# Kernel tuning notes

Measured on AMD Instinct MI355X. Metric: run time of the kernel, lower is better.

The kernel has to match this reference:

```python
import jax, jax.numpy as jnp
import numpy as np

H = 8  # number of heads


def setup_inputs() -> dict:
    key0 = jax.random.key(0)
    ks = jax.random.split(key0, 10)
    B, Lq, Lk = 2, 256, 512
    q_model = k_model = v_model = d_model = 512
    d_k = d_model // H
    s = 0.02
    return {
        "query": jax.random.normal(ks[0], (B, Lq, q_model), jnp.float32),
        "key": jax.random.normal(ks[1], (B, Lk, k_model), jnp.float32),
        "value": jax.random.normal(ks[2], (B, Lk, v_model), jnp.float32),
        "mask": jax.random.randint(ks[3], (B, Lk), 0, 2, jnp.int32),
        # weights stored as (in, out) so projection is x @ W
        "Wq": jax.random.normal(ks[4], (q_model, d_model), jnp.float32) * s,
        "Wk": jax.random.normal(ks[5], (k_model, d_model), jnp.float32) * s,
        "Wv": jax.random.normal(ks[6], (v_model, d_model), jnp.float32) * s,
        "Wo": jax.random.normal(ks[7], (d_model, d_model), jnp.float32) * s,
        "wa": jax.random.normal(ks[8], (d_k,), jnp.float32) * s,
    }


def reference(query, key, value, mask, Wq, Wk, Wv, Wo, wa):
    B, Lq, _ = query.shape
    Lk = key.shape[1]
    d_model = Wq.shape[1]
    d_k = d_model // H

    def split_heads(x, W, L):
        return (x @ W).reshape(B, L, H, d_k).transpose(0, 2, 1, 3)  # (B,H,L,dk)

    q = split_heads(query, Wq, Lq)
    k = split_heads(key, Wk, Lk)
    v = split_heads(value, Wv, Lk)

    # additive (Bahdanau) scores: tanh(q_i + k_j) . wa  -> (B,H,Lq,Lk)
    feats = jnp.tanh(q[:, :, :, None, :] + k[:, :, None, :, :])
    scores = jnp.einsum("bhqkd,d->bhqk", feats, wa)

    scores = jnp.where(mask[:, None, None, :] == 0, jnp.float32(-1e9), scores)
    weights = jax.nn.softmax(scores, axis=-1)

    x = jnp.einsum("bhqk,bhkd->bhqd", weights, v)
    x = x.transpose(0, 2, 1, 3).reshape(B, Lq, H * d_k)
    return x @ Wo
```

## Files before the change

kernel.cpp:

```cpp
#include <hip/hip_runtime.h>

#define NB 2
#define LQ 256
#define LK 512
#define DM 512
#define NH 8
#define C2F 2.885390081777927f
#define L2E 1.4426950408889634f

typedef __attribute__((ext_vector_type(8))) short short8;
typedef __attribute__((ext_vector_type(4))) float f32x4;

__device__ __forceinline__ ushort f2bf(float x) {
    unsigned int u = __float_as_uint(x);
    unsigned int r = (u + 0x7fffu + ((u >> 16) & 1u)) >> 16;
    return (ushort)r;
}
__device__ __forceinline__ float bf2f(ushort u) {
    return __uint_as_float(((unsigned int)u) << 16);
}

__global__ __launch_bounds__(256) void prep_kernel(
    const float* __restrict__ query, const float* __restrict__ key,
    const float* __restrict__ value, const int* __restrict__ mask,
    const float* __restrict__ Wq, const float* __restrict__ Wk,
    const float* __restrict__ Wv, const float* __restrict__ Wo,
    ushort* __restrict__ Ah, ushort* __restrict__ Al,
    ushort* __restrict__ Wth, ushort* __restrict__ Wtl,
    int* __restrict__ vidx, int* __restrict__ nvarr)
{
    __shared__ float T[32][33];
    const int blk = blockIdx.x;
    const int tid = threadIdx.x;

    if (blk < 1280) {
        int i = (blk * 256 + tid) * 4;
        const float* src;
        if (i < 262144)       src = query + i;
        else if (i < 786432)  src = key + (i - 262144);
        else                  src = value + (i - 786432);
        float4 x = *reinterpret_cast<const float4*>(src);
        ushort h0 = f2bf(x.x), h1 = f2bf(x.y), h2 = f2bf(x.z), h3 = f2bf(x.w);
        *reinterpret_cast<ushort4*>(&Ah[i]) = make_ushort4(h0, h1, h2, h3);
        *reinterpret_cast<ushort4*>(&Al[i]) = make_ushort4(
            f2bf(x.x - bf2f(h0)), f2bf(x.y - bf2f(h1)),
            f2bf(x.z - bf2f(h2)), f2bf(x.w - bf2f(h3)));
    } else if (blk < 2304) {
        const int bid2 = blk - 1280;
        const int widx = bid2 >> 8;
        const int kt = (bid2 >> 4) & 15, nt = bid2 & 15;
        const float* W = (widx == 0) ? Wq : (widx == 1) ? Wk : (widx == 2) ? Wv : Wo;
        const int rr = tid >> 3, c4 = tid & 7;
        float4 v = *reinterpret_cast<const float4*>(&W[(size_t)(kt * 32 + rr) * 512 + nt * 32 + c4 * 4]);
        T[c4 * 4 + 0][rr] = v.x;
        T[c4 * 4 + 1][rr] = v.y;
        T[c4 * 4 + 2][rr] = v.z;
        T[c4 * 4 + 3][rr] = v.w;
        __syncthreads();
        const int nr = tid >> 3, k4 = tid & 7;
        float x0 = T[nr][k4 * 4 + 0], x1 = T[nr][k4 * 4 + 1];
        float x2 = T[nr][k4 * 4 + 2], x3 = T[nr][k4 * 4 + 3];
        ushort h0 = f2bf(x0), h1 = f2bf(x1), h2 = f2bf(x2), h3 = f2bf(x3);
        size_t o = (size_t)widx * 262144 + (size_t)(nt * 32 + nr) * 512 + kt * 32 + k4 * 4;
        *reinterpret_cast<ushort4*>(&Wth[o]) = make_ushort4(h0, h1, h2, h3);
        *reinterpret_cast<ushort4*>(&Wtl[o]) = make_ushort4(
            f2bf(x0 - bf2f(h0)), f2bf(x1 - bf2f(h1)), f2bf(x2 - bf2f(h2)), f2bf(x3 - bf2f(h3)));
    } else {
        const int b = blk - 2304;
        if (tid < 64) {
            const int lane = tid;
            const int* mb = mask + b * LK;
            int base = 0;
            #pragma unroll
            for (int it = 0; it < 8; ++it) {
                int j = it * 64 + lane;
                bool m = mb[j] != 0;
                unsigned long long bal = __ballot(m);
                int pos = base + (int)__popcll(bal & ((1ull << lane) - 1ull));
                if (m) vidx[b * 512 + pos] = j;
                base += (int)__popcll(bal);
            }
            for (int j = base + lane; j < 512; j += 64) vidx[b * 512 + j] = 0;
            if (lane == 0) nvarr[b] = base;
        }
    }
}

__device__ __forceinline__ void wave_gemm16(
    const ushort* __restrict__ Ah, const ushort* __restrict__ Al, int arow0,
    const ushort* __restrict__ Bth, const ushort* __restrict__ Btl, int ncol0,
    float* __restrict__ C, int crow0, float scale, int lane)
{
    const int fr = lane & 15, k8 = (lane >> 4) * 8;
    const ushort* aph = Ah + (size_t)(arow0 + fr) * 512 + k8;
    const ushort* apl = Al + (size_t)(arow0 + fr) * 512 + k8;
    const ushort* bph = Bth + (size_t)(ncol0 + fr) * 512 + k8;
    const ushort* bpl = Btl + (size_t)(ncol0 + fr) * 512 + k8;
    f32x4 acc = (f32x4)0.0f;
    #pragma unroll 4
    for (int k0 = 0; k0 < 512; k0 += 32) {
        short8 a_h = *reinterpret_cast<const short8*>(aph + k0);
        short8 a_l = *reinterpret_cast<const short8*>(apl + k0);
        short8 b_h = *reinterpret_cast<const short8*>(bph + k0);
        short8 b_l = *reinterpret_cast<const short8*>(bpl + k0);
        acc = __builtin_amdgcn_mfma_f32_16x16x32_bf16(a_h, b_h, acc, 0, 0, 0);
        acc = __builtin_amdgcn_mfma_f32_16x16x32_bf16(a_h, b_l, acc, 0, 0, 0);
        acc = __builtin_amdgcn_mfma_f32_16x16x32_bf16(a_l, b_h, acc, 0, 0, 0);
    }
    #pragma unroll
    for (int i = 0; i < 4; ++i)
        C[(size_t)(crow0 + (lane >> 4) * 4 + i) * 512 + ncol0 + fr] = acc[i] * scale;
}

__global__ __launch_bounds__(256) void qkv_gemm_kernel(
    const ushort* __restrict__ Ah, const ushort* __restrict__ Al,
    const ushort* __restrict__ Wth, const ushort* __restrict__ Wtl,
    float* __restrict__ Qb, float* __restrict__ Kb, float* __restrict__ Vb)
{
    const int gw = (blockIdx.x * 256 + threadIdx.x) >> 6;
    const int lane = threadIdx.x & 63;
    const int mt = gw >> 5, nt = gw & 31;
    const ushort* bth; const ushort* btl; float* C; int crow0; float scale;
    if (mt < 32)      { bth = Wth;          btl = Wtl;          C = Qb; crow0 = mt * 16;        scale = C2F; }
    else if (mt < 96) { bth = Wth + 262144; btl = Wtl + 262144; C = Kb; crow0 = (mt - 32) * 16; scale = C2F; }
    else              { bth = Wth + 524288; btl = Wtl + 524288; C = Vb; crow0 = (mt - 96) * 16; scale = 1.0f; }
    wave_gemm16(Ah, Al, mt * 16, bth, btl, nt * 16, C, crow0, scale, lane);
}

__global__ __launch_bounds__(256) void out_gemm_kernel(
    const ushort* __restrict__ xh, const ushort* __restrict__ xl,
    const ushort* __restrict__ Woh, const ushort* __restrict__ Wol,
    float* __restrict__ out)
{
    const int gw = (blockIdx.x * 256 + threadIdx.x) >> 6;
    const int lane = threadIdx.x & 63;
    const int mt = gw >> 5, nt = gw & 31;
    wave_gemm16(xh, xl, mt * 16, Woh, Wol, nt * 16, out, mt * 16, 1.0f, lane);
}

#define SCOP(QV, KV, WV, U) { \
    float e_ = __builtin_amdgcn_exp2f((QV) + (KV)); \
    float r_ = __builtin_amdgcn_rcpf(1.0f + e_); \
    (U) = fmaf((WV), r_, (U)); }

__global__ __launch_bounds__(256) void attn_kernel(
    const float* __restrict__ Qb, const float* __restrict__ Kb,
    const float* __restrict__ Vb, const float* __restrict__ wa,
    const int* __restrict__ vidx, const int* __restrict__ nvarr,
    ushort* __restrict__ xh, ushort* __restrict__ xl)
{
    __shared__ float qs[2][64];
    __shared__ float was[64];
    __shared__ float wsm[2][512];
    __shared__ float red[2][8];
    __shared__ float xp[4][2][64];
    __shared__ int vlds[512];
    __shared__ int nv_s;

    const int tid = threadIdx.x;
    const int lane = tid & 63;
    const int w = tid >> 6;
    const int bid = blockIdx.x;
    const int qt = bid & 127;
    const int h = (bid >> 7) & 7;
    const int b = bid >> 10;
    const int q0 = qt * 2;

    if (tid < 128) {
        int r = tid >> 6, d = tid & 63;
        qs[r][d] = Qb[(size_t)(b * LQ + q0 + r) * DM + h * 64 + d];
    }
    if (tid < 64) was[tid] = wa[tid];
    vlds[tid] = vidx[b * 512 + tid];
    vlds[tid + 256] = vidx[b * 512 + tid + 256];
    if (tid == 0) nv_s = nvarr[b];
    __syncthreads();
    const int nv = nv_s;

    float swa = was[lane];
    #pragma unroll
    for (int off = 32; off > 0; off >>= 1) swa += __shfl_xor(swa, off);

    const float* Kh = Kb + ((size_t)b * LK) * DM + h * 64;
    float s[2][2];

    #pragma unroll
    for (int c = 0; c < 2; ++c) {
        const int sbase = c * 256 + w * 64;
        if (sbase >= nv) { s[0][c] = -1e9f; s[1][c] = -1e9f; continue; }
        const int slot = sbase + lane;
        const bool act = slot < nv;
        const int row = vlds[slot];
        const float* Kp = Kh + (size_t)row * DM;
        float u0 = 0.0f, u1 = 0.0f;
        #pragma unroll
        for (int db = 0; db < 8; ++db) {
            const int d0 = db * 8;
            float4 kA = *reinterpret_cast<const float4*>(&Kp[d0]);
            float4 kB = *reinterpret_cast<const float4*>(&Kp[d0 + 4]);
            float4 qA0 = *reinterpret_cast<const float4*>(&qs[0][d0]);
            float4 qB0 = *reinterpret_cast<const float4*>(&qs[0][d0 + 4]);
            float4 qA1 = *reinterpret_cast<const float4*>(&qs[1][d0]);
            float4 qB1 = *reinterpret_cast<const float4*>(&qs[1][d0 + 4]);
            float4 wA = *reinterpret_cast<const float4*>(&was[d0]);
            float4 wB = *reinterpret_cast<const float4*>(&was[d0 + 4]);
            SCOP(qA0.x, kA.x, wA.x, u0)  SCOP(qA1.x, kA.x, wA.x, u1)
            SCOP(qA0.y, kA.y, wA.y, u0)  SCOP(qA1.y, kA.y, wA.y, u1)
            SCOP(qA0.z, kA.z, wA.z, u0)  SCOP(qA1.z, kA.z, wA.z, u1)
            SCOP(qA0.w, kA.w, wA.w, u0)  SCOP(qA1.w, kA.w, wA.w, u1)
            SCOP(qB0.x, kB.x, wB.x, u0)  SCOP(qB1.x, kB.x, wB.x, u1)
            SCOP(qB0.y, kB.y, wB.y, u0)  SCOP(qB1.y, kB.y, wB.y, u1)
            SCOP(qB0.z, kB.z, wB.z, u0)  SCOP(qB1.z, kB.z, wB.z, u1)
            SCOP(qB0.w, kB.w, wB.w, u0)  SCOP(qB1.w, kB.w, wB.w, u1)
        }
        s[0][c] = act ? fmaf(-2.0f, u0, swa) : -1e9f;
        s[1][c] = act ? fmaf(-2.0f, u1, swa) : -1e9f;
    }

    #pragma unroll
    for (int r = 0; r < 2; ++r) {
        float mx = fmaxf(s[r][0], s[r][1]);
        #pragma unroll
        for (int off = 32; off > 0; off >>= 1) mx = fmaxf(mx, __shfl_xor(mx, off));
        if (lane == 0) red[r][w] = mx;
    }
    __syncthreads();
    float p[2][2];
    #pragma unroll
    for (int r = 0; r < 2; ++r) {
        float gmx = fmaxf(fmaxf(red[r][0], red[r][1]), fmaxf(red[r][2], red[r][3]));
        p[r][0] = __builtin_amdgcn_exp2f((s[r][0] - gmx) * L2E);
        p[r][1] = __builtin_amdgcn_exp2f((s[r][1] - gmx) * L2E);
        float sm = p[r][0] + p[r][1];
        #pragma unroll
        for (int off = 32; off > 0; off >>= 1) sm += __shfl_xor(sm, off);
        if (lane == 0) red[r][4 + w] = sm;
    }
    __syncthreads();
    #pragma unroll
    for (int r = 0; r < 2; ++r) {
        float tot = (red[r][4] + red[r][5]) + (red[r][6] + red[r][7]);
        float inv = __builtin_amdgcn_rcpf(tot);
        wsm[r][w * 64 + lane] = p[r][0] * inv;
        wsm[r][256 + w * 64 + lane] = p[r][1] * inv;
    }
    __syncthreads();

    const float* Vh = Vb + ((size_t)b * LK) * DM + h * 64;
    float o0 = 0.0f, o1 = 0.0f;
    const int ngr = (nv + 3) >> 2;
    for (int gi = w; gi < ngr; gi += 4) {
        const int sb = gi * 4;
        float4 w0 = *reinterpret_cast<const float4*>(&wsm[0][sb]);
        float4 w1 = *reinterpret_cast<const float4*>(&wsm[1][sb]);
        int j0 = vlds[sb + 0], j1 = vlds[sb + 1], j2 = vlds[sb + 2], j3 = vlds[sb + 3];
        float v0 = Vh[(size_t)j0 * DM + lane];
        float v1 = Vh[(size_t)j1 * DM + lane];
        float v2 = Vh[(size_t)j2 * DM + lane];
        float v3 = Vh[(size_t)j3 * DM + lane];
        o0 = fmaf(w0.x, v0, o0); o0 = fmaf(w0.y, v1, o0);
        o0 = fmaf(w0.z, v2, o0); o0 = fmaf(w0.w, v3, o0);
        o1 = fmaf(w1.x, v0, o1); o1 = fmaf(w1.y, v1, o1);
        o1 = fmaf(w1.z, v2, o1); o1 = fmaf(w1.w, v3, o1);
    }
    xp[w][0][lane] = o0;
    xp[w][1][lane] = o1;
    __syncthreads();
    if (w < 2) {
        const int r = w;
        float acc = (xp[0][r][lane] + xp[1][r][lane]) + (xp[2][r][lane] + xp[3][r][lane]);
        size_t oidx = (size_t)(b * LQ + q0 + r) * DM + h * 64 + lane;
        ushort hb = f2bf(acc);
        xh[oidx] = hb;
        xl[oidx] = f2bf(acc - bf2f(hb));
    }
}

extern "C" void kernel_launch(void* const* d_in, const int* in_sizes, int n_in,
                              void* d_out, int out_size, void* d_ws, size_t ws_size,
                              hipStream_t stream)
{
    const float* query = (const float*)d_in[0];
    const float* key   = (const float*)d_in[1];
    const float* value = (const float*)d_in[2];
    const int*   mask  = (const int*)d_in[3];
    const float* Wq    = (const float*)d_in[4];
    const float* Wk    = (const float*)d_in[5];
    const float* Wv    = (const float*)d_in[6];
    const float* Wo    = (const float*)d_in[7];
    const float* wa    = (const float*)d_in[8];
    float* out = (float*)d_out;

    char* W = (char*)d_ws;
    float*  Qb    = (float*)(W);
    float*  Kb    = (float*)(W + 1048576);
    float*  Vb    = (float*)(W + 3145728);
    ushort* Ah    = (ushort*)(W + 5242880);
    ushort* Al    = (ushort*)(W + 7864320);
    ushort* Wth   = (ushort*)(W + 10485760);
    ushort* Wtl   = (ushort*)(W + 12582912);
    ushort* xh    = (ushort*)(W + 14680064);
    ushort* xl    = (ushort*)(W + 15204352);
    int*    vidx  = (int*)(W + 15728640);
    int*    nvarr = (int*)(W + 15732736);

    prep_kernel<<<dim3(2306), 256, 0, stream>>>(query, key, value, mask,
                                                Wq, Wk, Wv, Wo, Ah, Al, Wth, Wtl, vidx, nvarr);
    qkv_gemm_kernel<<<dim3(1280), 256, 0, stream>>>(Ah, Al, Wth, Wtl, Qb, Kb, Vb);
    attn_kernel<<<dim3(2048), 256, 0, stream>>>(Qb, Kb, Vb, wa, vidx, nvarr, xh, xl);
    out_gemm_kernel<<<dim3(256), 256, 0, stream>>>(xh, xl, Wth + 786432, Wtl + 786432, out);
}
```

Before: 161.8 us.

## Tile GEMMs through LDS, compact K/V in epilogue, process four query rows per block

The projection and output GEMMs now compute 64x64 tiles per block, staging bf16 hi/lo operands in shared memory, where before each wave computed an independent 16x16 tile straight from global memory. The QKV GEMM epilogue scatters K and V rows directly into a compacted layout that holds only unmasked keys, using an inverse position map built in prep, so attention reads K and V contiguously with no index indirection. The attention kernel handles four query rows per block instead of two, reusing each loaded K/V row across more queries and halving the block count. The trade-offs are a much smaller GEMM grid (64 blocks for the output projection) and added synchronisation in the K loop.

```diff
diff --git a/kernel.cpp b/kernel.cpp
--- a/kernel.cpp
+++ b/kernel.cpp
@@ -5,6 +5,7 @@
 #define LK 512
 #define DM 512
 #define NH 8
+#define ROWS 4
 #define C2F 2.885390081777927f
 #define L2E 1.4426950408889634f
 
@@ -27,7 +28,7 @@
     const float* __restrict__ Wv, const float* __restrict__ Wo,
     ushort* __restrict__ Ah, ushort* __restrict__ Al,
     ushort* __restrict__ Wth, ushort* __restrict__ Wtl,
-    int* __restrict__ vidx, int* __restrict__ nvarr)
+    int* __restrict__ pinv, int* __restrict__ nvarr)
 {
     __shared__ float T[32][33];
     const int blk = blockIdx.x;
@@ -77,54 +78,109 @@
                 bool m = mb[j] != 0;
                 unsigned long long bal = __ballot(m);
                 int pos = base + (int)__popcll(bal & ((1ull << lane) - 1ull));
-                if (m) vidx[b * 512 + pos] = j;
+                pinv[b * 512 + j] = m ? pos : -1;
                 base += (int)__popcll(bal);
             }
-            for (int j = base + lane; j < 512; j += 64) vidx[b * 512 + j] = 0;
             if (lane == 0) nvarr[b] = base;
         }
     }
 }
 
-__device__ __forceinline__ void wave_gemm16(
+__device__ __forceinline__ void gemm64_acc(
     const ushort* __restrict__ Ah, const ushort* __restrict__ Al, int arow0,
-    const ushort* __restrict__ Bth, const ushort* __restrict__ Btl, int ncol0,
-    float* __restrict__ C, int crow0, float scale, int lane)
-{
-    const int fr = lane & 15, k8 = (lane >> 4) * 8;
-    const ushort* aph = Ah + (size_t)(arow0 + fr) * 512 + k8;
-    const ushort* apl = Al + (size_t)(arow0 + fr) * 512 + k8;
-    const ushort* bph = Bth + (size_t)(ncol0 + fr) * 512 + k8;
-    const ushort* bpl = Btl + (size_t)(ncol0 + fr) * 512 + k8;
-    f32x4 acc = (f32x4)0.0f;
-    #pragma unroll 4
+    const ushort* __restrict__ Bth, const ushort* __restrict__ Btl, int col0,
+    f32x4 (&acc)[2][2])
+{
+    __shared__ __align__(16) ushort AsH[64 * 40];
+    __shared__ __align__(16) ushort AsL[64 * 40];
+    __shared__ __align__(16) ushort BsH[64 * 40];
+    __shared__ __align__(16) ushort BsL[64 * 40];
+    const int tid = threadIdx.x;
+    const int lane = tid & 63;
+    const int w = tid >> 6, wr = w >> 1, wc = w & 1;
+    const int srow = tid >> 2, sk8 = (tid & 3) * 8;
+
+    #pragma unroll
+    for (int i = 0; i < 2; ++i)
+        #pragma unroll
+        for (int j = 0; j < 2; ++j) acc[i][j] = (f32x4)0.0f;
+
+    const int fr_row = (lane & 15), fk8 = (lane >> 4) * 8;
+
     for (int k0 = 0; k0 < 512; k0 += 32) {
-        short8 a_h = *reinterpret_cast<const short8*>(aph + k0);
-        short8 a_l = *reinterpret_cast<const short8*>(apl + k0);
-        short8 b_h = *reinterpret_cast<const short8*>(bph + k0);
-        short8 b_l = *reinterpret_cast<const short8*>(bpl + k0);
-        acc = __builtin_amdgcn_mfma_f32_16x16x32_bf16(a_h, b_h, acc, 0, 0, 0);
-        acc = __builtin_amdgcn_mfma_f32_16x16x32_bf16(a_h, b_l, acc, 0, 0, 0);
-        acc = __builtin_amdgcn_mfma_f32_16x16x32_bf16(a_l, b_h, acc, 0, 0, 0);
-    }
-    #pragma unroll
-    for (int i = 0; i < 4; ++i)
-        C[(size_t)(crow0 + (lane >> 4) * 4 + i) * 512 + ncol0 + fr] = acc[i] * scale;
+        short8 gah = *reinterpret_cast<const short8*>(&Ah[(size_t)(arow0 + srow) * 512 + k0 + sk8]);
+        short8 gal = *reinterpret_cast<const short8*>(&Al[(size_t)(arow0 + srow) * 512 + k0 + sk8]);
+        short8 gbh = *reinterpret_cast<const short8*>(&Bth[(size_t)(col0 + srow) * 512 + k0 + sk8]);
+        short8 gbl = *reinterpret_cast<const short8*>(&Btl[(size_t)(col0 + srow) * 512 + k0 + sk8]);
+        __syncthreads();
+        *reinterpret_cast<short8*>(&AsH[srow * 40 + sk8]) = gah;
+        *reinterpret_cast<short8*>(&AsL[srow * 40 + sk8]) = gal;
+        *reinterpret_cast<short8*>(&BsH[srow * 40 + sk8]) = gbh;
+        *reinterpret_cast<short8*>(&BsL[srow * 40 + sk8]) = gbl;
+        __syncthreads();
+        short8 ah[2], al[2], bh[2], bl[2];
+        #pragma unroll
+        for (int fr = 0; fr < 2; ++fr) {
+            int r = wr * 32 + fr * 16 + fr_row;
+            ah[fr] = *reinterpret_cast<const short8*>(&AsH[r * 40 + fk8]);
+            al[fr] = *reinterpret_cast<const short8*>(&AsL[r * 40 + fk8]);
+        }
+        #pragma unroll
+        for (int fc = 0; fc < 2; ++fc) {
+            int n = wc * 32 + fc * 16 + fr_row;
+            bh[fc] = *reinterpret_cast<const short8*>(&BsH[n * 40 + fk8]);
+            bl[fc] = *reinterpret_cast<const short8*>(&BsL[n * 40 + fk8]);
+        }
+        #pragma unroll
+        for (int fr = 0; fr < 2; ++fr)
+            #pragma unroll
+            for (int fc = 0; fc < 2; ++fc) {
+                acc[fr][fc] = __builtin_amdgcn_mfma_f32_16x16x32_bf16(ah[fr], bh[fc], acc[fr][fc], 0, 0, 0);
+                acc[fr][fc] = __builtin_amdgcn_mfma_f32_16x16x32_bf16(ah[fr], bl[fc], acc[fr][fc], 0, 0, 0);
+                acc[fr][fc] = __builtin_amdgcn_mfma_f32_16x16x32_bf16(al[fr], bh[fc], acc[fr][fc], 0, 0, 0);
+            }
+    }
 }
 
 __global__ __launch_bounds__(256) void qkv_gemm_kernel(
     const ushort* __restrict__ Ah, const ushort* __restrict__ Al,
     const ushort* __restrict__ Wth, const ushort* __restrict__ Wtl,
-    float* __restrict__ Qb, float* __restrict__ Kb, float* __restrict__ Vb)
-{
-    const int gw = (blockIdx.x * 256 + threadIdx.x) >> 6;
+    const int* __restrict__ pinv,
+    float* __restrict__ Qb, float* __restrict__ Kc, float* __restrict__ Vc)
+{
+    const int rb = blockIdx.y, cb = blockIdx.x;
+    const int row0 = rb * 64, col0 = cb * 64;
+    const ushort* bth; const ushort* btl;
+    if (rb < 8)       { bth = Wth;          btl = Wtl; }
+    else if (rb < 24) { bth = Wth + 262144; btl = Wtl + 262144; }
+    else              { bth = Wth + 524288; btl = Wtl + 524288; }
+    f32x4 acc[2][2];
+    gemm64_acc(Ah, Al, row0, bth, btl, col0, acc);
     const int lane = threadIdx.x & 63;
-    const int mt = gw >> 5, nt = gw & 31;
-    const ushort* bth; const ushort* btl; float* C; int crow0; float scale;
-    if (mt < 32)      { bth = Wth;          btl = Wtl;          C = Qb; crow0 = mt * 16;        scale = C2F; }
-    else if (mt < 96) { bth = Wth + 262144; btl = Wtl + 262144; C = Kb; crow0 = (mt - 32) * 16; scale = C2F; }
-    else              { bth = Wth + 524288; btl = Wtl + 524288; C = Vb; crow0 = (mt - 96) * 16; scale = 1.0f; }
-    wave_gemm16(Ah, Al, mt * 16, bth, btl, nt * 16, C, crow0, scale, lane);
+    const int w = threadIdx.x >> 6, wr = w >> 1, wc = w & 1;
+    #pragma unroll
+    for (int fr = 0; fr < 2; ++fr)
+        #pragma unroll
+        for (int fc = 0; fc < 2; ++fc)
+            #pragma unroll
+            for (int i = 0; i < 4; ++i) {
+                int r = row0 + wr * 32 + fr * 16 + (lane >> 4) * 4 + i;
+                int c = col0 + wc * 32 + fc * 16 + (lane & 15);
+                float v = acc[fr][fc][i];
+                if (r < 512) {
+                    Qb[(size_t)r * 512 + c] = v * C2F;
+                } else if (r < 1536) {
+                    int rk = r - 512;
+                    int pos = pinv[rk];
+                    if (pos >= 0)
+                        Kc[(size_t)((rk >> 9) * 512 + pos) * 512 + c] = v * C2F;
+                } else {
+                    int rv = r - 1536;
+                    int pos = pinv[rv];
+                    if (pos >= 0)
+                        Vc[(size_t)((rv >> 9) * 512 + pos) * 512 + c] = v;
+                }
+            }
 }
 
 __global__ __launch_bounds__(256) void out_gemm_kernel(
@@ -132,10 +188,21 @@
     const ushort* __restrict__ Woh, const ushort* __restrict__ Wol,
     float* __restrict__ out)
 {
-    const int gw = (blockIdx.x * 256 + threadIdx.x) >> 6;
+    const int row0 = blockIdx.y * 64, col0 = blockIdx.x * 64;
+    f32x4 acc[2][2];
+    gemm64_acc(xh, xl, row0, Woh, Wol, col0, acc);
     const int lane = threadIdx.x & 63;
-    const int mt = gw >> 5, nt = gw & 31;
-    wave_gemm16(xh, xl, mt * 16, Woh, Wol, nt * 16, out, mt * 16, 1.0f, lane);
+    const int w = threadIdx.x >> 6, wr = w >> 1, wc = w & 1;
+    #pragma unroll
+    for (int fr = 0; fr < 2; ++fr)
+        #pragma unroll
+        for (int fc = 0; fc < 2; ++fc)
+            #pragma unroll
+            for (int i = 0; i < 4; ++i) {
+                int r = row0 + wr * 32 + fr * 16 + (lane >> 4) * 4 + i;
+                int c = col0 + wc * 32 + fc * 16 + (lane & 15);
+                out[(size_t)r * 512 + c] = acc[fr][fc][i];
+            }
 }
 
 #define SCOP(QV, KV, WV, U) { \
@@ -144,35 +211,32 @@
     (U) = fmaf((WV), r_, (U)); }
 
 __global__ __launch_bounds__(256) void attn_kernel(
-    const float* __restrict__ Qb, const float* __restrict__ Kb,
-    const float* __restrict__ Vb, const float* __restrict__ wa,
-    const int* __restrict__ vidx, const int* __restrict__ nvarr,
+    const float* __restrict__ Qb, const float* __restrict__ Kc,
+    const float* __restrict__ Vc, const float* __restrict__ wa,
+    const int* __restrict__ nvarr,
     ushort* __restrict__ xh, ushort* __restrict__ xl)
 {
-    __shared__ float qs[2][64];
+    __shared__ float qs[ROWS][64];
     __shared__ float was[64];
-    __shared__ float wsm[2][512];
-    __shared__ float red[2][8];
-    __shared__ float xp[4][2][64];
-    __shared__ int vlds[512];
+    __shared__ float wsm[ROWS][512];
+    __shared__ float red[ROWS][8];
+    __shared__ float xp[4][ROWS][64];
     __shared__ int nv_s;
 
     const int tid = threadIdx.x;
     const int lane = tid & 63;
     const int w = tid >> 6;
     const int bid = blockIdx.x;
-    const int qt = bid & 127;
-    const int h = (bid >> 7) & 7;
-    const int b = bid >> 10;
-    const int q0 = qt * 2;
-
-    if (tid < 128) {
+    const int qt = bid & 63;
+    const int h = (bid >> 6) & 7;
+    const int b = bid >> 9;
+    const int q0 = qt * ROWS;
+
+    {
         int r = tid >> 6, d = tid & 63;
         qs[r][d] = Qb[(size_t)(b * LQ + q0 + r) * DM + h * 64 + d];
     }
     if (tid < 64) was[tid] = wa[tid];
-    vlds[tid] = vidx[b * 512 + tid];
-    vlds[tid + 256] = vidx[b * 512 + tid + 256];
     if (tid == 0) nv_s = nvarr[b];
     __syncthreads();
     const int nv = nv_s;
@@ -181,53 +245,58 @@
     #pragma unroll
     for (int off = 32; off > 0; off >>= 1) swa += __shfl_xor(swa, off);
 
-    const float* Kh = Kb + ((size_t)b * LK) * DM + h * 64;
-    float s[2][2];
+    const float* Kh = Kc + ((size_t)b * LK) * DM + h * 64;
+    float s[ROWS][2];
 
     #pragma unroll
     for (int c = 0; c < 2; ++c) {
         const int sbase = c * 256 + w * 64;
-        if (sbase >= nv) { s[0][c] = -1e9f; s[1][c] = -1e9f; continue; }
+        if (sbase >= nv) {
+            #pragma unroll
+            for (int r = 0; r < ROWS; ++r) s[r][c] = -1e9f;
+            continue;
+        }
         const int slot = sbase + lane;
         const bool act = slot < nv;
-        const int row = vlds[slot];
-        const float* Kp = Kh + (size_t)row * DM;
-        float u0 = 0.0f, u1 = 0.0f;
+        const float* Kp = Kh + (size_t)slot * DM;
+        float u[ROWS] = {0.0f, 0.0f, 0.0f, 0.0f};
         #pragma unroll
         for (int db = 0; db < 8; ++db) {
             const int d0 = db * 8;
             float4 kA = *reinterpret_cast<const float4*>(&Kp[d0]);
             float4 kB = *reinterpret_cast<const float4*>(&Kp[d0 + 4]);
-            float4 qA0 = *reinterpret_cast<const float4*>(&qs[0][d0]);
-            float4 qB0 = *reinterpret_cast<const float4*>(&qs[0][d0 + 4]);
-            float4 qA1 = *reinterpret_cast<const float4*>(&qs[1][d0]);
-            float4 qB1 = *reinterpret_cast<const float4*>(&qs[1][d0 + 4]);
             float4 wA = *reinterpret_cast<const float4*>(&was[d0]);
             float4 wB = *reinterpret_cast<const float4*>(&was[d0 + 4]);
-            SCOP(qA0.x, kA.x, wA.x, u0)  SCOP(qA1.x, kA.x, wA.x, u1)
-            SCOP(qA0.y, kA.y, wA.y, u0)  SCOP(qA1.y, kA.y, wA.y, u1)
-            SCOP(qA0.z, kA.z, wA.z, u0)  SCOP(qA1.z, kA.z, wA.z, u1)
-            SCOP(qA0.w, kA.w, wA.w, u0)  SCOP(qA1.w, kA.w, wA.w, u1)
-            SCOP(qB0.x, kB.x, wB.x, u0)  SCOP(qB1.x, kB.x, wB.x, u1)
-            SCOP(qB0.y, kB.y, wB.y, u0)  SCOP(qB1.y, kB.y, wB.y, u1)
-            SCOP(qB0.z, kB.z, wB.z, u0)  SCOP(qB1.z, kB.z, wB.z, u1)
-            SCOP(qB0.w, kB.w, wB.w, u0)  SCOP(qB1.w, kB.w, wB.w, u1)
-        }
-        s[0][c] = act ? fmaf(-2.0f, u0, swa) : -1e9f;
-        s[1][c] = act ? fmaf(-2.0f, u1, swa) : -1e9f;
-    }
-
-    #pragma unroll
-    for (int r = 0; r < 2; ++r) {
+            #pragma unroll
+            for (int r = 0; r < ROWS; ++r) {
+                float4 qA = *reinterpret_cast<const float4*>(&qs[r][d0]);
+                float4 qB = *reinterpret_cast<const float4*>(&qs[r][d0 + 4]);
+                SCOP(qA.x, kA.x, wA.x, u[r])
+                SCOP(qA.y, kA.y, wA.y, u[r])
+                SCOP(qA.z, kA.z, wA.z, u[r])
+                SCOP(qA.w, kA.w, wA.w, u[r])
+                SCOP(qB.x, kB.x, wB.x, u[r])
+                SCOP(qB.y, kB.y, wB.y, u[r])
+                SCOP(qB.z, kB.z, wB.z, u[r])
+                SCOP(qB.w, kB.w, wB.w, u[r])
+            }
+        }
+        #pragma unroll
+        for (int r = 0; r < ROWS; ++r)
+            s[r][c] = act ? fmaf(-2.0f, u[r], swa) : -1e9f;
+    }
+
+    #pragma unroll
+    for (int r = 0; r < ROWS; ++r) {
         float mx = fmaxf(s[r][0], s[r][1]);
         #pragma unroll
         for (int off = 32; off > 0; off >>= 1) mx = fmaxf(mx, __shfl_xor(mx, off));
         if (lane == 0) red[r][w] = mx;
     }
     __syncthreads();
-    float p[2][2];
-    #pragma unroll
-    for (int r = 0; r < 2; ++r) {
+    float p[ROWS][2];
+    #pragma unroll
+    for (int r = 0; r < ROWS; ++r) {
         float gmx = fmaxf(fmaxf(red[r][0], red[r][1]), fmaxf(red[r][2], red[r][3]));
         p[r][0] = __builtin_amdgcn_exp2f((s[r][0] - gmx) * L2E);
         p[r][1] = __builtin_amdgcn_exp2f((s[r][1] - gmx) * L2E);
@@ -238,7 +307,7 @@
     }
     __syncthreads();
     #pragma unroll
-    for (int r = 0; r < 2; ++r) {
+    for (int r = 0; r < ROWS; ++r) {
         float tot = (red[r][4] + red[r][5]) + (red[r][6] + red[r][7]);
         float inv = __builtin_amdgcn_rcpf(tot);
         wsm[r][w * 64 + lane] = p[r][0] * inv;
@@ -246,27 +315,32 @@
     }
     __syncthreads();
 
-    const float* Vh = Vb + ((size_t)b * LK) * DM + h * 64;
-    float o0 = 0.0f, o1 = 0.0f;
+    const float* Vh = Vc + ((size_t)b * LK) * DM + h * 64;
+    float o[ROWS] = {0.0f, 0.0f, 0.0f, 0.0f};
     const int ngr = (nv + 3) >> 2;
     for (int gi = w; gi < ngr; gi += 4) {
         const int sb = gi * 4;
         float4 w0 = *reinterpret_cast<const float4*>(&wsm[0][sb]);
         float4 w1 = *reinterpret_cast<const float4*>(&wsm[1][sb]);
-        int j0 = vlds[sb + 0], j1 = vlds[sb + 1], j2 = vlds[sb + 2], j3 = vlds[sb + 3];
-        float v0 = Vh[(size_t)j0 * DM + lane];
-        float v1 = Vh[(size_t)j1 * DM + lane];
-        float v2 = Vh[(size_t)j2 * DM + lane];
-        float v3 = Vh[(size_t)j3 * DM + lane];
-        o0 = fmaf(w0.x, v0, o0); o0 = fmaf(w0.y, v1, o0);
-        o0 = fmaf(w0.z, v2, o0); o0 = fmaf(w0.w, v3, o0);
-        o1 = fmaf(w1.x, v0, o1); o1 = fmaf(w1.y, v1, o1);
-        o1 = fmaf(w1.z, v2, o1); o1 = fmaf(w1.w, v3, o1);
-    }
-    xp[w][0][lane] = o0;
-    xp[w][1][lane] = o1;
-    __syncthreads();
-    if (w < 2) {
+        float4 w2 = *reinterpret_cast<const float4*>(&wsm[2][sb]);
+        float4 w3 = *reinterpret_cast<const float4*>(&wsm[3][sb]);
+        float v0 = Vh[(size_t)(sb + 0) * DM + lane];
+        float v1 = Vh[(size_t)(sb + 1) * DM + lane];
+        float v2 = Vh[(size_t)(sb + 2) * DM + lane];
+        float v3 = Vh[(size_t)(sb + 3) * DM + lane];
+        o[0] = fmaf(w0.x, v0, o[0]); o[0] = fmaf(w0.y, v1, o[0]);
+        o[0] = fmaf(w0.z, v2, o[0]); o[0] = fmaf(w0.w, v3, o[0]);
+        o[1] = fmaf(w1.x, v0, o[1]); o[1] = fmaf(w1.y, v1, o[1]);
+        o[1] = fmaf(w1.z, v2, o[1]); o[1] = fmaf(w1.w, v3, o[1]);
+        o[2] = fmaf(w2.x, v0, o[2]); o[2] = fmaf(w2.y, v1, o[2]);
+        o[2] = fmaf(w2.z, v2, o[2]); o[2] = fmaf(w2.w, v3, o[2]);
+        o[3] = fmaf(w3.x, v0, o[3]); o[3] = fmaf(w3.y, v1, o[3]);
+        o[3] = fmaf(w3.z, v2, o[3]); o[3] = fmaf(w3.w, v3, o[3]);
+    }
+    #pragma unroll
+    for (int r = 0; r < ROWS; ++r) xp[w][r][lane] = o[r];
+    __syncthreads();
+    {
         const int r = w;
         float acc = (xp[0][r][lane] + xp[1][r][lane]) + (xp[2][r][lane] + xp[3][r][lane]);
         size_t oidx = (size_t)(b * LQ + q0 + r) * DM + h * 64 + lane;
@@ -293,20 +367,20 @@
 
     char* W = (char*)d_ws;
     float*  Qb    = (float*)(W);
-    float*  Kb    = (float*)(W + 1048576);
-    float*  Vb    = (float*)(W + 3145728);
+    float*  Kc    = (float*)(W + 1048576);
+    float*  Vc    = (float*)(W + 3145728);
     ushort* Ah    = (ushort*)(W + 5242880);
     ushort* Al    = (ushort*)(W + 7864320);
     ushort* Wth   = (ushort*)(W + 10485760);
     ushort* Wtl   = (ushort*)(W + 12582912);
     ushort* xh    = (ushort*)(W + 14680064);
     ushort* xl    = (ushort*)(W + 15204352);
-    int*    vidx  = (int*)(W + 15728640);
+    int*    pinv  = (int*)(W + 15728640);
     int*    nvarr = (int*)(W + 15732736);
 
     prep_kernel<<<dim3(2306), 256, 0, stream>>>(query, key, value, mask,
-                                                Wq, Wk, Wv, Wo, Ah, Al, Wth, Wtl, vidx, nvarr);
-    qkv_gemm_kernel<<<dim3(1280), 256, 0, stream>>>(Ah, Al, Wth, Wtl, Qb, Kb, Vb);
-    attn_kernel<<<dim3(2048), 256, 0, stream>>>(Qb, Kb, Vb, wa, vidx, nvarr, xh, xl);
-    out_gemm_kernel<<<dim3(256), 256, 0, stream>>>(xh, xl, Wth + 786432, Wtl + 786432, out);
-}
+                                                Wq, Wk, Wv, Wo, Ah, Al, Wth, Wtl, pinv, nvarr);
+    qkv_gemm_kernel<<<dim3(8, 40), 256, 0, stream>>>(Ah, Al, Wth, Wtl, pinv, Qb, Kc, Vc);
+    attn_kernel<<<dim3(1024), 256, 0, stream>>>(Qb, Kc, Vc, wa, nvarr, xh, xl);
+    out_gemm_kernel<<<dim3(8, 8), 256, 0, stream>>>(xh, xl, Wth + 786432, Wtl + 786432, out);
+}
```

Result: faster. 136.4 us (-15.7%).
